# Optimization experiments

Measured on AMD Instinct MI355X. Metric: run time of the kernel, lower is better.

The kernel has to match this reference:

```python
import jax, jax.numpy as jnp
import numpy as np

BN_EPS = 1e-5
TEMPERATURE = 256 ** 0.5  # sqrt(c2), since cv3 = ScaledDotProductAttention(c2)


def conv_bn_silu(x, w, gamma, beta, mean, var):
    # Conv2d(k=3, s=1, pad='same', bias=False) -> BatchNorm2d (running stats) -> SiLU
    y = jax.lax.conv_general_dilated(
        x, w, window_strides=(1, 1), padding='SAME',
        dimension_numbers=('NCHW', 'OIHW', 'NCHW'))
    scale = (gamma / jnp.sqrt(var + BN_EPS))[None, :, None, None]
    shift = (beta - mean * gamma / jnp.sqrt(var + BN_EPS))[None, :, None, None]
    y = y * scale + shift
    return y * jax.nn.sigmoid(y)  # SiLU


def setup_inputs() -> dict:
    key = jax.random.key(0)
    ks = jax.random.split(key, 8)
    B, C, H, W = 16, 256, 64, 64
    Ch = 128  # hidden channels c_ = int(c2 * e)
    x = jax.random.normal(ks[0], (B, C, H, W), dtype=jnp.float32)
    w1 = jax.random.normal(ks[1], (Ch, C, 3, 3), dtype=jnp.float32) * 0.05
    g1 = jnp.ones((Ch,), jnp.float32) + 0.1 * jax.random.normal(ks[2], (Ch,), dtype=jnp.float32)
    b1 = 0.1 * jax.random.normal(ks[3], (Ch,), dtype=jnp.float32)
    m1 = 0.1 * jax.random.normal(ks[4], (Ch,), dtype=jnp.float32)
    v1 = jnp.ones((Ch,), jnp.float32) + 0.5 * jax.random.uniform(ks[5], (Ch,), dtype=jnp.float32)
    w2 = jax.random.normal(ks[6], (C, Ch, 3, 3), dtype=jnp.float32) * 0.05
    g2 = jnp.ones((C,), jnp.float32)
    b2 = jnp.zeros((C,), jnp.float32)
    m2 = 0.1 * jax.random.normal(ks[7], (C,), dtype=jnp.float32)
    v2 = jnp.ones((C,), jnp.float32) + 0.5 * jax.random.uniform(jax.random.fold_in(key, 99), (C,), dtype=jnp.float32)
    return {"x": x, "w1": w1, "g1": g1, "b1": b1, "m1": m1, "v1": v1,
            "w2": w2, "g2": g2, "b2": b2, "m2": m2, "v2": v2}


def reference(x, w1, g1, b1, m1, v1, w2, g2, b2, m2, v2):
    y = conv_bn_silu(x, w1, g1, b1, m1, v1)       # [B, 128, H, W]
    y = conv_bn_silu(y, w2, g2, b2, m2, v2)       # [B, 256, H, W]
    B, C, H, W = y.shape
    q = y.reshape(B, C, H * W)                    # q = k^T = v, all views of y
    # channel-channel attention: scores [B, C, C]
    scores = jnp.einsum('bcn,bdn->bcd', q / TEMPERATURE, q)
    attn = jax.nn.softmax(scores, axis=-1)        # dropout is identity in eval
    out = jnp.einsum('bcd,bdn->bcn', attn, q).reshape(B, C, H, W)
    return x + out  # shortcut: c1 == c2
```

## Files before the change

### kernel.cpp

```cpp
#include <hip/hip_runtime.h>
#include <math.h>

#define BB 16
#define C1 256
#define CHD 128
#define NN 4096
#define INV_T (1.0f/16.0f)

typedef _Float16 half8 __attribute__((ext_vector_type(8)));
typedef __attribute__((ext_vector_type(4))) float f32x4;
typedef __attribute__((ext_vector_type(16))) float f32x16;

__device__ inline unsigned short f2h(float f) {
    _Float16 h = (_Float16)f;
    return __builtin_bit_cast(unsigned short, h);
}

#define GLDS(g, l) __builtin_amdgcn_global_load_lds(                              \
    (const __attribute__((address_space(1))) unsigned int*)(g),                   \
    (__attribute__((address_space(3))) unsigned int*)(l), 16, 0, 0)

__global__ __launch_bounds__(256) void nchw_to_nhwc_f16(
    const float* __restrict__ x, unsigned short* __restrict__ xh, int C)
{
    const int c0 = blockIdx.x * 64;
    const int hp = blockIdx.y;
    const int b  = blockIdx.z;

    if (hp == 0 || hp == 65) {
        for (int idx = threadIdx.x; idx < 1024; idx += 256) {
            int w = idx >> 4, cq = (idx & 15) * 4;
            ushort4 z; z.x = z.y = z.z = z.w = 0;
            *(ushort4*)&xh[(((size_t)b * 66 + hp) * 64 + w) * C + c0 + cq] = z;
        }
        return;
    }
    const int h = hp - 1;
    __shared__ float ts[64][65];
    for (int idx = threadIdx.x; idx < 4096; idx += 256) {
        int cl = idx >> 6, w = idx & 63;
        ts[cl][w] = x[(((size_t)b * C + c0 + cl) * 64 + h) * 64 + w];
    }
    __syncthreads();
    for (int idx = threadIdx.x; idx < 1024; idx += 256) {
        int w = idx >> 4, cq = (idx & 15) * 4;
        ushort4 o;
        o.x = f2h(ts[cq + 0][w]); o.y = f2h(ts[cq + 1][w]);
        o.z = f2h(ts[cq + 2][w]); o.w = f2h(ts[cq + 3][w]);
        *(ushort4*)&xh[(((size_t)b * 66 + hp) * 64 + w) * C + c0 + cq] = o;
    }
}

__global__ __launch_bounds__(256) void pack_w_kernel(
    const float* __restrict__ w, unsigned short* __restrict__ wT, int Cout, int Cin)
{
    int idx = blockIdx.x * 256 + threadIdx.x;
    int total = Cout * Cin * 9;
    if (idx >= total) return;
    int ci = idx % Cin; int t = idx / Cin; int co = t % Cout; int kk = t / Cout;
    wT[idx] = f2h(w[((size_t)co * Cin + ci) * 9 + kk]);
}

__global__ __launch_bounds__(256) void zero_y1h_pads(unsigned short* __restrict__ y1h)
{
    int idx = blockIdx.x * 256 + threadIdx.x;
    int b = idx >> 12;
    int row = ((idx >> 11) & 1) ? 65 : 0;
    int inner = idx & 2047;
    ushort4 z; z.x = z.y = z.z = z.w = 0;
    *(ushort4*)&y1h[(((size_t)b * 66 + row) * 64) * 128 + inner * 4] = z;
}

__global__ __launch_bounds__(512, 4) void conv_mfma_kernel(
    const unsigned short* __restrict__ xh, const unsigned short* __restrict__ wT,
    const float* __restrict__ gamma, const float* __restrict__ beta,
    const float* __restrict__ mean, const float* __restrict__ var,
    unsigned short* __restrict__ outNHWC,
    unsigned short* __restrict__ yhi, unsigned short* __restrict__ yhiT,
    int Cin, int Cout)
{
    const int tid  = threadIdx.x;
    const int wid  = tid >> 6;
    const int lane = tid & 63;
    const int l31  = lane & 31;
    const int hi   = lane >> 5;
    const int coBase = blockIdx.x * 64;
    const int h0     = blockIdx.y * 8;
    const int b      = blockIdx.z;

    __shared__ unsigned short xs[2][10560];
    __shared__ unsigned short ws[2][9216];
    __shared__ float bnsc[64], bnsh[64];

    if (tid < 64) {
        int co = coBase + tid;
        float sc = gamma[co] * rsqrtf(var[co] + 1e-5f);
        bnsc[tid] = sc;
        bnsh[tid] = beta[co] - mean[co] * sc;
    }
    if (tid < 160) {
        int r    = tid >> 4;
        int rem  = tid & 15;
        int buf  = rem >> 3;
        int rem2 = rem & 7;
        int col  = (rem2 >> 2) ? 65 : 0;
        int part = rem2 & 3;
        ushort4 z; z.x = z.y = z.z = z.w = 0;
        *(ushort4*)&xs[buf][(r * 66 + col) * 16 + part * 4] = z;
    }

    auto stage = [&](int sel, int ck) {
        const int ci0 = ck << 4;
        for (int it = wid; it < 38; it += 8) {
            if (it < 18) {
                int row = it * 32 + (lane >> 1);
                int kk  = row >> 6;
                int co  = row & 63;
                const unsigned short* g =
                    wT + (((size_t)kk * Cout + coBase + co) * Cin + ci0 + (lane & 1) * 8);
                GLDS(g, &ws[sel][it * 512]);
            } else {
                int j  = it - 18;
                int r  = j >> 1;
                int hf = j & 1;
                int colL = hf * 32 + (lane >> 1);
                const unsigned short* g =
                    xh + ((((size_t)b * 66 + h0 + r) * 64 + colL) * Cin + ci0 + (lane & 1) * 8);
                GLDS(g, &xs[sel][(r * 66 + 1 + hf * 32) * 16]);
            }
        }
    };

    stage(0, 0);
    __syncthreads();

    f32x16 acc[2][2] = {};

    const int nCk = Cin >> 4;
    int sel = 0;
    for (int ck = 0; ck < nCk; ck++) {
        if (ck + 1 < nCk) stage(sel ^ 1, ck + 1);

        const unsigned short* wsb = &ws[sel][0];
        const unsigned short* xsb = &xs[sel][0];
#pragma unroll
        for (int kk = 0; kk < 9; kk++) {
            const int kh = kk / 3, kw = kk % 3;
            half8 a0 = *(const half8*)&wsb[(kk * 64 +      l31) * 16 + hi * 8];
            half8 a1 = *(const half8*)&wsb[(kk * 64 + 32 + l31) * 16 + hi * 8];
            const unsigned short* xr = &xsb[((wid + kh) * 66 + l31 + kw) * 16 + hi * 8];
            half8 b0 = *(const half8*)xr;
            half8 b1 = *(const half8*)&xr[32 * 16];
            acc[0][0] = __builtin_amdgcn_mfma_f32_32x32x16_f16(a0, b0, acc[0][0], 0, 0, 0);
            acc[0][1] = __builtin_amdgcn_mfma_f32_32x32x16_f16(a0, b1, acc[0][1], 0, 0, 0);
            acc[1][0] = __builtin_amdgcn_mfma_f32_32x32x16_f16(a1, b0, acc[1][0], 0, 0, 0);
            acc[1][1] = __builtin_amdgcn_mfma_f32_32x32x16_f16(a1, b1, acc[1][1], 0, 0, 0);
        }
        __syncthreads();
        sel ^= 1;
    }

    const int orow = h0 + wid;
    if (outNHWC) {
#pragma unroll
        for (int mi = 0; mi < 2; mi++)
#pragma unroll
            for (int ni = 0; ni < 2; ni++) {
                f32x16 a = acc[mi][ni];
                int w = ni * 32 + l31;
                size_t rowbase = (((size_t)b * 66 + orow + 1) * 64 + w) * Cout + coBase;
#pragma unroll
                for (int rq = 0; rq < 4; rq++) {
                    int c0 = mi * 32 + rq * 8 + hi * 4;
                    ushort4 o; unsigned short* op = (unsigned short*)&o;
#pragma unroll
                    for (int r = 0; r < 4; r++) {
                        float t = a[rq * 4 + r] * bnsc[c0 + r] + bnsh[c0 + r];
                        op[r] = f2h(t / (1.f + __expf(-t)));
                    }
                    *(ushort4*)&outNHWC[rowbase + c0] = o;
                }
            }
    } else {
#pragma unroll
        for (int mi = 0; mi < 2; mi++)
#pragma unroll
            for (int ni = 0; ni < 2; ni++) {
                f32x16 a = acc[mi][ni];
                int w = ni * 32 + l31;
#pragma unroll
                for (int rq = 0; rq < 4; rq++) {
                    int c0 = mi * 32 + rq * 8 + hi * 4;
                    ushort4 o; unsigned short* op = (unsigned short*)&o;
#pragma unroll
                    for (int r = 0; r < 4; r++) {
                        float t = a[rq * 4 + r] * bnsc[c0 + r] + bnsh[c0 + r];
                        float s = t / (1.f + __expf(-t));
                        op[r] = f2h(s);
                        yhi[(((size_t)b * Cout + coBase + c0 + r) * 64 + orow) * 64 + w] = op[r];
                    }
                    *(ushort4*)&yhiT[((size_t)b * 4096 + (size_t)orow * 64 + w) * Cout
                                     + coBase + c0] = o;
                }
            }
    }
}

__global__ __launch_bounds__(256) void scores_mfma_kernel(
    const unsigned short* __restrict__ yhi, float* __restrict__ scores)
{
    static const int TI[10] = {0,0,0,0,1,1,1,2,2,3};
    static const int TJ[10] = {0,1,2,3,1,2,3,2,3,3};
    const int b  = blockIdx.z;
    const int ti = TI[blockIdx.x], tj = TJ[blockIdx.x];
    const int cB = ti * 64;
    const int dB = tj * 64;
    const int tid  = threadIdx.x;
    const int wid  = tid >> 6;
    const int lane = tid & 63;
    const int ln   = lane & 15;
    const int q    = lane >> 4;
    const int wm   = wid >> 1, wn = wid & 1;

    __shared__ unsigned short As[64 * 128];
    __shared__ unsigned short Bs[64 * 128];

    const int rl = lane >> 4;
    const int gl = lane & 15;

    f32x4 acc[2][2] = {};

    for (int ck = 0; ck < 32; ck++) {
        const int n0 = ck * 128;
        for (int it = wid; it < 32; it += 4) {
            const int tile = it >> 4;
            const int j = it & 15;
            const int r = j * 4 + rl;
            const int gq = gl ^ (r & 7);
            const int rowAbs = (tile ? dB : cB) + r;
            const unsigned short* g =
                yhi + ((size_t)b * 256 + rowAbs) * 4096 + n0 + gq * 8;
            GLDS(g, (tile ? Bs : As) + j * 512);
        }
        __syncthreads();

#pragma unroll
        for (int kwin = 0; kwin < 4; kwin++) {
            half8 ah[2], bh[2];
#pragma unroll
            for (int mi = 0; mi < 2; mi++) {
                int row = wm * 32 + mi * 16 + ln;
                ah[mi] = *(const half8*)&As[row * 128 + ((kwin * 4 + q) ^ (ln & 7)) * 8];
            }
#pragma unroll
            for (int ni = 0; ni < 2; ni++) {
                int row = wn * 32 + ni * 16 + ln;
                bh[ni] = *(const half8*)&Bs[row * 128 + ((kwin * 4 + q) ^ (ln & 7)) * 8];
            }
#pragma unroll
            for (int mi = 0; mi < 2; mi++)
#pragma unroll
                for (int ni = 0; ni < 2; ni++)
                    acc[mi][ni] = __builtin_amdgcn_mfma_f32_16x16x32_f16(
                        ah[mi], bh[ni], acc[mi][ni], 0, 0, 0);
        }
        __syncthreads();
    }

#pragma unroll
    for (int mi = 0; mi < 2; mi++)
#pragma unroll
        for (int ni = 0; ni < 2; ni++) {
            f32x4 a = acc[mi][ni];
            float vals[4];
            vals[0] = a.x * INV_T; vals[1] = a.y * INV_T;
            vals[2] = a.z * INV_T; vals[3] = a.w * INV_T;
            int c0 = cB + wm * 32 + mi * 16 + q * 4;
            int d  = dB + wn * 32 + ni * 16 + ln;
#pragma unroll
            for (int r = 0; r < 4; r++)
                scores[((size_t)b * C1 + c0 + r) * C1 + d] = vals[r];
            if (ti != tj) {
                float4 tv = {vals[0], vals[1], vals[2], vals[3]};
                *(float4*)&scores[((size_t)b * C1 + d) * C1 + c0] = tv;
            }
        }
}

__global__ __launch_bounds__(64) void softmax_kernel(
    const float* __restrict__ scores, unsigned short* __restrict__ attn16)
{
    const int row = blockIdx.x;
    const float* p = scores + (size_t)row * C1;
    const int lane = threadIdx.x;

    float4 v = ((const float4*)p)[lane];
    float m = fmaxf(fmaxf(v.x, v.y), fmaxf(v.z, v.w));
#pragma unroll
    for (int off = 32; off >= 1; off >>= 1)
        m = fmaxf(m, __shfl_xor(m, off, 64));

    float4 e;
    e.x = expf(v.x - m); e.y = expf(v.y - m);
    e.z = expf(v.z - m); e.w = expf(v.w - m);
    float s = e.x + e.y + e.z + e.w;
#pragma unroll
    for (int off = 32; off >= 1; off >>= 1)
        s += __shfl_xor(s, off, 64);
    float inv = 1.f / s;
    ushort4 o;
    o.x = f2h(e.x * inv); o.y = f2h(e.y * inv);
    o.z = f2h(e.z * inv); o.w = f2h(e.w * inv);
    *(ushort4*)&attn16[(size_t)row * C1 + lane * 4] = o;
}

__global__ __launch_bounds__(256) void out_mfma_kernel(
    const unsigned short* __restrict__ attn16, const unsigned short* __restrict__ yhiT,
    const float* __restrict__ x, float* __restrict__ out)
{
    const int b  = blockIdx.z;
    const int cB = blockIdx.y * 64;
    const int nB = blockIdx.x * 128;
    const int tid  = threadIdx.x;
    const int wid  = tid >> 6;
    const int lane = tid & 63;
    const int ln   = lane & 15;
    const int q    = lane >> 4;
    const int wm   = wid >> 1, wn = wid & 1;

    __shared__ unsigned short As[64 * 64];
    __shared__ unsigned short Bs[128 * 64];

    const int r8 = lane >> 3;
    const int gq = (lane & 7) ^ r8;

    f32x4 acc[2][4] = {};

    for (int ck = 0; ck < 4; ck++) {
        const int d0 = ck * 64;
        for (int it = wid; it < 24; it += 4) {
            if (it < 8) {
                const unsigned short* g =
                    attn16 + ((size_t)b * 256 + cB + it * 8 + r8) * 256 + d0 + gq * 8;
                GLDS(g, As + it * 512);
            } else {
                int j = it - 8;
                const unsigned short* g =
                    yhiT + ((size_t)b * 4096 + nB + j * 8 + r8) * 256 + d0 + gq * 8;
                GLDS(g, Bs + j * 512);
            }
        }
        __syncthreads();

#pragma unroll
        for (int kwin = 0; kwin < 2; kwin++) {
            const int cc = (((kwin * 4 + q) ^ (ln & 7))) * 8;
            half8 af[2], bfr[4];
#pragma unroll
            for (int mi = 0; mi < 2; mi++)
                af[mi] = *(const half8*)&As[(wm * 32 + mi * 16 + ln) * 64 + cc];
#pragma unroll
            for (int ni = 0; ni < 4; ni++)
                bfr[ni] = *(const half8*)&Bs[(wn * 64 + ni * 16 + ln) * 64 + cc];
#pragma unroll
            for (int mi = 0; mi < 2; mi++)
#pragma unroll
                for (int ni = 0; ni < 4; ni++)
                    acc[mi][ni] = __builtin_amdgcn_mfma_f32_16x16x32_f16(
                        af[mi], bfr[ni], acc[mi][ni], 0, 0, 0);
        }
        __syncthreads();
    }

#pragma unroll
    for (int mi = 0; mi < 2; mi++)
#pragma unroll
        for (int ni = 0; ni < 4; ni++) {
            f32x4 a = acc[mi][ni];
            float vals[4] = {a.x, a.y, a.z, a.w};
#pragma unroll
            for (int r = 0; r < 4; r++) {
                int c = cB + wm * 32 + mi * 16 + q * 4 + r;
                int n = nB + wn * 64 + ni * 16 + ln;
                size_t o = ((size_t)b * C1 + c) * NN + n;
                out[o] = x[o] + vals[r];
            }
        }
}

extern "C" void kernel_launch(void* const* d_in, const int* in_sizes, int n_in,
                              void* d_out, int out_size, void* d_ws, size_t ws_size,
                              hipStream_t stream)
{
    const float* x  = (const float*)d_in[0];
    const float* w1 = (const float*)d_in[1];
    const float* g1 = (const float*)d_in[2];
    const float* b1 = (const float*)d_in[3];
    const float* m1 = (const float*)d_in[4];
    const float* v1 = (const float*)d_in[5];
    const float* w2 = (const float*)d_in[6];
    const float* g2 = (const float*)d_in[7];
    const float* b2 = (const float*)d_in[8];
    const float* m2 = (const float*)d_in[9];
    const float* v2 = (const float*)d_in[10];
    float* out = (float*)d_out;

    unsigned short* xh   = (unsigned short*)d_ws;
    unsigned short* y1h  = xh  + (size_t)17301504;
    unsigned short* wt1  = y1h + (size_t)8650752;
    unsigned short* wt2  = wt1 + (size_t)294912;
    unsigned short* yhiT = wt2 + (size_t)294912;
    unsigned short* yhi  = xh;
    float*          sc   = (float*)y1h;
    unsigned short* attn16 = (unsigned short*)(sc + 1048576);

    nchw_to_nhwc_f16<<<dim3(C1 / 64, 66, BB), 256, 0, stream>>>(x, xh, C1);
    pack_w_kernel<<<(9 * CHD * C1 + 255) / 256, 256, 0, stream>>>(w1, wt1, CHD, C1);
    pack_w_kernel<<<(9 * C1 * CHD + 255) / 256, 256, 0, stream>>>(w2, wt2, C1, CHD);
    zero_y1h_pads<<<256, 256, 0, stream>>>(y1h);

    conv_mfma_kernel<<<dim3(CHD / 64, 8, BB), 512, 0, stream>>>(
        xh, wt1, g1, b1, m1, v1, y1h, nullptr, nullptr, C1, CHD);
    conv_mfma_kernel<<<dim3(C1 / 64, 8, BB), 512, 0, stream>>>(
        y1h, wt2, g2, b2, m2, v2, nullptr, yhi, yhiT, CHD, C1);

    scores_mfma_kernel<<<dim3(10, 1, BB), 256, 0, stream>>>(yhi, sc);
    softmax_kernel<<<dim3(BB * C1), 64, 0, stream>>>(sc, attn16);
    out_mfma_kernel<<<dim3(NN / 128, 4, BB), 256, 0, stream>>>(attn16, yhiT, x, out);
}
```

Baseline: 343.7 us.

## Use channel-chunked blocked layouts and LDS-staged coalesced conv epilogue stores

Activations and packed weights move to a blocked layout where each group of 16 channels is contiguous per spatial position. Each global_load_lds in the conv and output GEMM then reads a contiguous run instead of strided 32-byte pieces. The conv epilogue writes results into swizzled LDS and then stores 16-byte vectors in the new blocked layout, replacing scattered 8-byte NHWC stores. The cost is an extra LDS round trip and barriers in the epilogue, and every consumer of these buffers must agree on the new layout.

Result: faster. 326.1 us (-5.1%).

```diff
diff --git a/kernel.cpp b/kernel.cpp
--- a/kernel.cpp
+++ b/kernel.cpp
@@ -26,12 +26,14 @@
     const int c0 = blockIdx.x * 64;
     const int hp = blockIdx.y;
     const int b  = blockIdx.z;
+    const int nCk = C >> 4;
 
     if (hp == 0 || hp == 65) {
         for (int idx = threadIdx.x; idx < 1024; idx += 256) {
             int w = idx >> 4, cq = (idx & 15) * 4;
             ushort4 z; z.x = z.y = z.z = z.w = 0;
-            *(ushort4*)&xh[(((size_t)b * 66 + hp) * 64 + w) * C + c0 + cq] = z;
+            *(ushort4*)&xh[((((size_t)b * nCk + (c0 >> 4) + (cq >> 4)) * 66 + hp) * 64 + w) * 16
+                           + (cq & 15)] = z;
         }
         return;
     }
@@ -47,7 +49,8 @@
         ushort4 o;
         o.x = f2h(ts[cq + 0][w]); o.y = f2h(ts[cq + 1][w]);
         o.z = f2h(ts[cq + 2][w]); o.w = f2h(ts[cq + 3][w]);
-        *(ushort4*)&xh[(((size_t)b * 66 + hp) * 64 + w) * C + c0 + cq] = o;
+        *(ushort4*)&xh[((((size_t)b * nCk + (c0 >> 4) + (cq >> 4)) * 66 + hp) * 64 + w) * 16
+                       + (cq & 15)] = o;
     }
 }
 
@@ -58,17 +61,20 @@
     int total = Cout * Cin * 9;
     if (idx >= total) return;
     int ci = idx % Cin; int t = idx / Cin; int co = t % Cout; int kk = t / Cout;
-    wT[idx] = f2h(w[((size_t)co * Cin + ci) * 9 + kk]);
+    wT[((((size_t)(ci >> 4)) * 9 + kk) * Cout + co) * 16 + (ci & 15)] =
+        f2h(w[((size_t)co * Cin + ci) * 9 + kk]);
 }
 
 __global__ __launch_bounds__(256) void zero_y1h_pads(unsigned short* __restrict__ y1h)
 {
     int idx = blockIdx.x * 256 + threadIdx.x;
-    int b = idx >> 12;
-    int row = ((idx >> 11) & 1) ? 65 : 0;
-    int inner = idx & 2047;
+    int b   = idx >> 12;
+    int ck  = (idx >> 9) & 7;
+    int row = ((idx >> 8) & 1) ? 65 : 0;
+    int w   = (idx >> 2) & 63;
+    int qtr = idx & 3;
     ushort4 z; z.x = z.y = z.z = z.w = 0;
-    *(ushort4*)&y1h[(((size_t)b * 66 + row) * 64) * 128 + inner * 4] = z;
+    *(ushort4*)&y1h[((((size_t)b * 8 + ck) * 66 + row) * 64 + w) * 16 + qtr * 4] = z;
 }
 
 __global__ __launch_bounds__(512, 4) void conv_mfma_kernel(
@@ -87,9 +93,9 @@
     const int coBase = blockIdx.x * 64;
     const int h0     = blockIdx.y * 8;
     const int b      = blockIdx.z;
-
-    __shared__ unsigned short xs[2][10560];
-    __shared__ unsigned short ws[2][9216];
+    const int nCk    = Cin >> 4;
+
+    __shared__ __align__(16) unsigned short smem[39552];
     __shared__ float bnsc[64], bnsh[64];
 
     if (tid < 64) {
@@ -99,34 +105,30 @@
         bnsh[tid] = beta[co] - mean[co] * sc;
     }
     if (tid < 160) {
-        int r    = tid >> 4;
-        int rem  = tid & 15;
-        int buf  = rem >> 3;
-        int rem2 = rem & 7;
-        int col  = (rem2 >> 2) ? 65 : 0;
-        int part = rem2 & 3;
+        int cell = tid >> 2;
+        int part = tid & 3;
+        int buf  = cell & 1;
+        int col  = ((cell >> 1) & 1) ? 65 : 0;
+        int r    = cell >> 2;
         ushort4 z; z.x = z.y = z.z = z.w = 0;
-        *(ushort4*)&xs[buf][(r * 66 + col) * 16 + part * 4] = z;
+        *(ushort4*)&smem[buf * 10560 + (r * 66 + col) * 16 + part * 4] = z;
     }
 
     auto stage = [&](int sel, int ck) {
-        const int ci0 = ck << 4;
+        unsigned short* wsd = smem + 21120 + sel * 9216;
+        unsigned short* xsd = smem + sel * 10560;
         for (int it = wid; it < 38; it += 8) {
             if (it < 18) {
-                int row = it * 32 + (lane >> 1);
-                int kk  = row >> 6;
-                int co  = row & 63;
+                int kk = it >> 1, h = it & 1;
                 const unsigned short* g =
-                    wT + (((size_t)kk * Cout + coBase + co) * Cin + ci0 + (lane & 1) * 8);
-                GLDS(g, &ws[sel][it * 512]);
+                    wT + (((size_t)ck * 9 + kk) * Cout + coBase + h * 32) * 16 + lane * 8;
+                GLDS(g, wsd + (kk * 64 + h * 32) * 16);
             } else {
-                int j  = it - 18;
-                int r  = j >> 1;
-                int hf = j & 1;
-                int colL = hf * 32 + (lane >> 1);
+                int j = it - 18;
+                int r = j >> 1, hf = j & 1;
                 const unsigned short* g =
-                    xh + ((((size_t)b * 66 + h0 + r) * 64 + colL) * Cin + ci0 + (lane & 1) * 8);
-                GLDS(g, &xs[sel][(r * 66 + 1 + hf * 32) * 16]);
+                    xh + ((((size_t)b * nCk + ck) * 66 + h0 + r) * 64 + hf * 32) * 16 + lane * 8;
+                GLDS(g, xsd + (r * 66 + 1 + hf * 32) * 16);
             }
         }
     };
@@ -136,13 +138,12 @@
 
     f32x16 acc[2][2] = {};
 
-    const int nCk = Cin >> 4;
     int sel = 0;
     for (int ck = 0; ck < nCk; ck++) {
         if (ck + 1 < nCk) stage(sel ^ 1, ck + 1);
 
-        const unsigned short* wsb = &ws[sel][0];
-        const unsigned short* xsb = &xs[sel][0];
+        const unsigned short* wsb = smem + 21120 + sel * 9216;
+        const unsigned short* xsb = smem + sel * 10560;
 #pragma unroll
         for (int kk = 0; kk < 9; kk++) {
             const int kh = kk / 3, kw = kk % 3;
@@ -161,48 +162,52 @@
     }
 
     const int orow = h0 + wid;
-    if (outNHWC) {
-#pragma unroll
-        for (int mi = 0; mi < 2; mi++)
-#pragma unroll
-            for (int ni = 0; ni < 2; ni++) {
-                f32x16 a = acc[mi][ni];
-                int w = ni * 32 + l31;
-                size_t rowbase = (((size_t)b * 66 + orow + 1) * 64 + w) * Cout + coBase;
-#pragma unroll
-                for (int rq = 0; rq < 4; rq++) {
-                    int c0 = mi * 32 + rq * 8 + hi * 4;
-                    ushort4 o; unsigned short* op = (unsigned short*)&o;
-#pragma unroll
-                    for (int r = 0; r < 4; r++) {
-                        float t = a[rq * 4 + r] * bnsc[c0 + r] + bnsh[c0 + r];
-                        op[r] = f2h(t / (1.f + __expf(-t)));
-                    }
-                    *(ushort4*)&outNHWC[rowbase + c0] = o;
+    const bool isConv1 = (outNHWC != nullptr);
+
+    __syncthreads();
+
+#pragma unroll
+    for (int mi = 0; mi < 2; mi++)
+#pragma unroll
+        for (int ni = 0; ni < 2; ni++) {
+            f32x16 a = acc[mi][ni];
+            int w = ni * 32 + l31;
+            int swz = ((l31 + wid) & 7) << 3;
+#pragma unroll
+            for (int rq = 0; rq < 4; rq++) {
+                int c0 = mi * 32 + rq * 8 + hi * 4;
+                ushort4 o; unsigned short* op = (unsigned short*)&o;
+#pragma unroll
+                for (int r = 0; r < 4; r++) {
+                    float t = a[rq * 4 + r] * bnsc[c0 + r] + bnsh[c0 + r];
+                    float s = t / (1.f + __expf(-t));
+                    op[r] = f2h(s);
+                    if (!isConv1)
+                        yhi[(((size_t)b * Cout + coBase + c0 + r) * 64 + orow) * 64 + w] = op[r];
                 }
-            }
-    } else {
-#pragma unroll
-        for (int mi = 0; mi < 2; mi++)
-#pragma unroll
-            for (int ni = 0; ni < 2; ni++) {
-                f32x16 a = acc[mi][ni];
-                int w = ni * 32 + l31;
-#pragma unroll
-                for (int rq = 0; rq < 4; rq++) {
-                    int c0 = mi * 32 + rq * 8 + hi * 4;
-                    ushort4 o; unsigned short* op = (unsigned short*)&o;
-#pragma unroll
-                    for (int r = 0; r < 4; r++) {
-                        float t = a[rq * 4 + r] * bnsc[c0 + r] + bnsh[c0 + r];
-                        float s = t / (1.f + __expf(-t));
-                        op[r] = f2h(s);
-                        yhi[(((size_t)b * Cout + coBase + c0 + r) * 64 + orow) * 64 + w] = op[r];
-                    }
-                    *(ushort4*)&yhiT[((size_t)b * 4096 + (size_t)orow * 64 + w) * Cout
-                                     + coBase + c0] = o;
-                }
-            }
+                *(ushort4*)&smem[wid * 4096 + w * 64 + (c0 ^ swz)] = o;
+            }
+        }
+    __syncthreads();
+
+    const int ckB = blockIdx.x * 4;
+    const int nCkOut = Cout >> 4;
+#pragma unroll
+    for (int j = 0; j < 8; j++) {
+        int g   = j * 512 + tid;
+        int s   = g & 1;
+        int w   = (g >> 1) & 63;
+        int row = (g >> 7) & 7;
+        int ck  = g >> 10;
+        uint4 v = *(const uint4*)&smem[row * 4096 + w * 64 +
+                     (((ck * 2 + s) * 8) ^ (((w + row) & 7) << 3))];
+        if (isConv1) {
+            *(uint4*)&outNHWC[((((size_t)b * nCkOut + ckB + ck) * 66 + h0 + row + 1) * 64 + w) * 16
+                              + s * 8] = v;
+        } else {
+            *(uint4*)&yhiT[(((size_t)b * nCkOut + ckB + ck) * 4096 + (size_t)(h0 + row) * 64 + w) * 16
+                           + s * 8] = v;
+        }
     }
 }
 
@@ -329,7 +334,7 @@
     const int wm   = wid >> 1, wn = wid & 1;
 
     __shared__ unsigned short As[64 * 64];
-    __shared__ unsigned short Bs[128 * 64];
+    __shared__ unsigned short Bs[4 * 128 * 16];
 
     const int r8 = lane >> 3;
     const int gq = (lane & 7) ^ r8;
@@ -345,9 +350,10 @@
                 GLDS(g, As + it * 512);
             } else {
                 int j = it - 8;
+                int u = j >> 2, part = j & 3;
                 const unsigned short* g =
-                    yhiT + ((size_t)b * 4096 + nB + j * 8 + r8) * 256 + d0 + gq * 8;
-                GLDS(g, Bs + j * 512);
+                    yhiT + (((size_t)b * 16 + ck * 4 + u) * 4096 + nB + part * 32) * 16 + lane * 8;
+                GLDS(g, Bs + (u * 128 + part * 32) * 16);
             }
         }
         __syncthreads();
@@ -355,13 +361,16 @@
 #pragma unroll
         for (int kwin = 0; kwin < 2; kwin++) {
             const int cc = (((kwin * 4 + q) ^ (ln & 7))) * 8;
+            const int gK = kwin * 4 + q;
             half8 af[2], bfr[4];
 #pragma unroll
             for (int mi = 0; mi < 2; mi++)
                 af[mi] = *(const half8*)&As[(wm * 32 + mi * 16 + ln) * 64 + cc];
 #pragma unroll
-            for (int ni = 0; ni < 4; ni++)
-                bfr[ni] = *(const half8*)&Bs[(wn * 64 + ni * 16 + ln) * 64 + cc];
+            for (int ni = 0; ni < 4; ni++) {
+                int row = wn * 64 + ni * 16 + ln;
+                bfr[ni] = *(const half8*)&Bs[(gK >> 1) * 2048 + row * 16 + (gK & 1) * 8];
+            }
 #pragma unroll
             for (int mi = 0; mi < 2; mi++)
 #pragma unroll
```
